# Kernel optimization log

Measured on AMD Instinct MI355X. Metric: run time of the kernel, lower is better.

## Reference

```python
import jax, jax.numpy as jnp
import numpy as np
import math

WINDOW = 14
NUM_HEADS = 12


def setup_inputs() -> dict:
    key = jax.random.key(0)
    k1, k2, k3 = jax.random.split(key, 3)
    B, H, W, C = 8, 80, 80, 768
    x = jax.random.normal(k1, (B, H * W, C), dtype=jnp.float32)
    Wqkv = jax.random.normal(k2, (C, 3 * C), dtype=jnp.float32) * 0.02
    Wproj = jax.random.normal(k3, (C, C), dtype=jnp.float32) * 0.02
    bproj = jnp.zeros((C,), dtype=jnp.float32)
    return {"x": x, "Wqkv": Wqkv, "Wproj": Wproj, "bproj": bproj, "H": H, "W": W}


def reference(x, Wqkv, Wproj, bproj, H, W):
    B, N, C = x.shape
    w = WINDOW
    nh = NUM_HEADS
    hd = C // nh
    scale = hd ** (-0.5)
    Hp = math.ceil(H / w) * w
    Wp = math.ceil(W / w) * w
    nH, nW = Hp // w, Wp // w
    L, Nw = nH * nW, w * w

    qkv = x @ Wqkv                                   # [B, N, 3C]
    grid = qkv.reshape(B, H, W, 3 * C)
    grid = jnp.pad(grid, ((0, 0), (0, Hp - H), (0, Wp - W), (0, 0)))
    # window partition: [B, nH, w, nW, w, 3C] -> [B, L, Nw, 3, nh, hd]
    win = grid.reshape(B, nH, w, nW, w, 3 * C).transpose(0, 1, 3, 2, 4, 5)
    win = win.reshape(B, L, Nw, 3, nh, hd)
    q = win[:, :, :, 0].transpose(0, 1, 3, 2, 4)     # [B, L, nh, Nw, hd]
    k = win[:, :, :, 1].transpose(0, 1, 3, 2, 4)
    v = win[:, :, :, 2].transpose(0, 1, 3, 2, 4)

    attn = jnp.einsum('blhnd,blhmd->blhnm', q, k) * scale
    attn = jax.nn.softmax(attn, axis=-1)
    out = jnp.einsum('blhnm,blhmd->blhnd', attn, v)  # [B, L, nh, Nw, hd]

    # window merge (fold with stride == kernel, non-overlapping)
    out = out.transpose(0, 1, 3, 2, 4).reshape(B, nH, nW, w, w, C)
    out = out.transpose(0, 1, 3, 2, 4, 5).reshape(B, Hp, Wp, C)
    out = out[:, :H, :W, :].reshape(B, N, C)
    return out @ Wproj + bproj
```

## Files before the change

### kernel.cpp

```cpp
#include <hip/hip_runtime.h>

typedef unsigned short u16;
typedef __attribute__((ext_vector_type(4))) float f32x4;
typedef __attribute__((ext_vector_type(8))) short bf16x8;

__device__ __forceinline__ u16 f2bf(float f) {
  unsigned u = __builtin_bit_cast(unsigned, f);
  u += 0x7FFFu + ((u >> 16) & 1u);
  return (u16)(u >> 16);
}

__device__ __forceinline__ void load16(const void* g, void* l) {
  __builtin_amdgcn_global_load_lds((const __attribute__((address_space(1))) void*)g,
                                   (__attribute__((address_space(3))) void*)l, 16, 0, 0);
}

#define LDS_ORDER() do { __builtin_amdgcn_s_waitcnt(0xC07F); asm volatile("" ::: "memory"); } while (0)


__global__ void cvt_x(const float* __restrict__ in, u16* __restrict__ out, int n4) {
  int i = blockIdx.x * 256 + threadIdx.x;
  if (i < n4) {
    float4 v = ((const float4*)in)[i];
    ushort4 o;
    o.x = f2bf(v.x); o.y = f2bf(v.y); o.z = f2bf(v.z); o.w = f2bf(v.w);
    ((ushort4*)out)[i] = o;
  }
}

__global__ void cvt_wt(const float* __restrict__ W, u16* __restrict__ Wt, int K, int N) {
  int idx = blockIdx.x * 256 + threadIdx.x;
  if (idx < N * K) {
    int n = idx / K, k = idx - n * K;
    Wt[idx] = f2bf(W[(size_t)k * N + n]);
  }
}


__global__ __launch_bounds__(256) void gemm_qkv(const u16* __restrict__ A,
                                                const u16* __restrict__ Bt,
                                                u16* __restrict__ qkvP,
                                                int M, int N, int K) {
  __shared__ __align__(16) u16 lA[128 * 32];
  __shared__ __align__(16) u16 lB[128 * 32];
  const int t = threadIdx.x;
  const int lane = t & 63, wave = t >> 6;
  const int wm = wave & 1, wn = wave >> 1;
  const int col = lane & 15, quad = lane >> 4;
  const int bn = blockIdx.x, bm = blockIdx.y;

  const int rowA = t >> 2;
  const int ke = (t & 3) * 8;
  const u16* gA = A + (size_t)(bm * 128 + rowA) * K + ke;
  const u16* gB = Bt + (size_t)(bn * 128 + rowA) * K + ke;
  u16* dA = &lA[t * 8];
  u16* dB = &lB[t * 8];
  const size_t stride64 = (size_t)64 * K;

  f32x4 acc[4][4] = {};

  for (int k0 = 0; k0 < K; k0 += 32) {
    load16(gA + k0, dA);
    load16(gA + k0 + stride64, dA + 2048);
    load16(gB + k0, dB);
    load16(gB + k0 + stride64, dB + 2048);
    __syncthreads();
    bf16x8 af[4], bfr[4];
#pragma unroll
    for (int i = 0; i < 4; i++)
      af[i] = *(const bf16x8*)&lA[(wm * 64 + i * 16 + col) * 32 + quad * 8];
#pragma unroll
    for (int j = 0; j < 4; j++)
      bfr[j] = *(const bf16x8*)&lB[(wn * 64 + j * 16 + col) * 32 + quad * 8];
#pragma unroll
    for (int i = 0; i < 4; i++)
#pragma unroll
      for (int j = 0; j < 4; j++)
        acc[i][j] = __builtin_amdgcn_mfma_f32_16x16x32_bf16(af[i], bfr[j], acc[i][j], 0, 0, 0);
    __syncthreads();
  }

  const int c0 = bn * 128 + wn * 64;
  const int mat = c0 / 768;
  const int hh = (c0 - mat * 768) >> 6;
  const int r0 = bm * 128 + wm * 64 + quad * 4;
#pragma unroll
  for (int i = 0; i < 4; i++) {
#pragma unroll
    for (int r = 0; r < 4; r++) {
      int row = r0 + i * 16 + r;
      int bb = row / 6400;
      int rem = row - bb * 6400;
      int y = rem / 80, x = rem - (rem / 80) * 80;
      int wy = y / 14, wx = x / 14;
      int iy = y - wy * 14, ix = x - wx * 14;
      int win = wy * 6 + wx;
      int kidx = iy * 14 + ix;
      size_t base = ((size_t)((bb * 36 + win) * 3 + mat) * 12 + hh) * 12544 + (size_t)kidx * 64;
#pragma unroll
      for (int j = 0; j < 4; j++)
        qkvP[base + j * 16 + col] = f2bf(acc[i][j][r]);
    }
  }
}


__global__ __launch_bounds__(256) void gemm_proj(const u16* __restrict__ A,
                                                 const u16* __restrict__ Bt,
                                                 float* __restrict__ C,
                                                 const float* __restrict__ bias,
                                                 int M, int N, int K) {
  __shared__ __align__(16) u16 lA[128 * 32];
  __shared__ __align__(16) u16 lB[128 * 32];
  const int t = threadIdx.x;
  const int lane = t & 63, wave = t >> 6;
  const int wm = wave & 1, wn = wave >> 1;
  const int col = lane & 15, quad = lane >> 4;
  const int bn = blockIdx.x, bm = blockIdx.y;

  const int rowA = t >> 2;
  const int ke = (t & 3) * 8;
  const u16* gA = A + (size_t)(bm * 128 + rowA) * K + ke;
  const u16* gB = Bt + (size_t)(bn * 128 + rowA) * K + ke;
  u16* dA = &lA[t * 8];
  u16* dB = &lB[t * 8];
  const size_t stride64 = (size_t)64 * K;

  f32x4 acc[4][4] = {};

  for (int k0 = 0; k0 < K; k0 += 32) {
    load16(gA + k0, dA);
    load16(gA + k0 + stride64, dA + 2048);
    load16(gB + k0, dB);
    load16(gB + k0 + stride64, dB + 2048);
    __syncthreads();
    bf16x8 af[4], bfr[4];
#pragma unroll
    for (int i = 0; i < 4; i++)
      af[i] = *(const bf16x8*)&lA[(wm * 64 + i * 16 + col) * 32 + quad * 8];
#pragma unroll
    for (int j = 0; j < 4; j++)
      bfr[j] = *(const bf16x8*)&lB[(wn * 64 + j * 16 + col) * 32 + quad * 8];
#pragma unroll
    for (int i = 0; i < 4; i++)
#pragma unroll
      for (int j = 0; j < 4; j++)
        acc[i][j] = __builtin_amdgcn_mfma_f32_16x16x32_bf16(af[i], bfr[j], acc[i][j], 0, 0, 0);
    __syncthreads();
  }

  const int r0 = bm * 128 + wm * 64 + quad * 4;
  const int c0 = bn * 128 + wn * 64 + col;
  float bv[4];
#pragma unroll
  for (int j = 0; j < 4; j++) bv[j] = bias[c0 + j * 16];
#pragma unroll
  for (int i = 0; i < 4; i++)
#pragma unroll
    for (int j = 0; j < 4; j++)
#pragma unroll
      for (int r = 0; r < 4; r++)
        C[(size_t)(r0 + i * 16 + r) * N + (c0 + j * 16)] = acc[i][j][r] + bv[j];
}


__global__ __launch_bounds__(256) void win_attn(const u16* __restrict__ qkvP,
                                                u16* __restrict__ out) {
  __shared__ __align__(16) u16 sK[2 * 208 * 32];
  __shared__ __align__(16) u16 sVt[7 * 64 * 32];
  __shared__ __align__(16) u16 sVrow[200 * 64];

  const int h = blockIdx.x;
  const int win = blockIdx.y;
  const int b = blockIdx.z;
  const int wy = win / 6, wx = win - wy * 6;
  const int y0 = wy * 14, x0 = wx * 14;
  const int t = threadIdx.x, wave = t >> 6, lane = t & 63;
  const int colq = lane & 15, quad = lane >> 4;

  const size_t bwin = (size_t)(b * 36 + win) * 3;
  const u16* qbase = qkvP + ((bwin + 0) * 12 + h) * 12544;
  const u16* kbase = qkvP + ((bwin + 1) * 12 + h) * 12544;
  const u16* vbase = qkvP + ((bwin + 2) * 12 + h) * 12544;

  for (int s = t; s < 3264; s += 256) {
    if (s < 1664) {
      int half = s / 832;
      int rem = s - half * 832;
      int row = rem >> 2, e = rem & 3;
      int srow = row < 196 ? row : 0;
      load16(kbase + srow * 64 + half * 32 + e * 8, (u16*)sK + s * 8);
    } else {
      int s2 = s - 1664;
      load16(vbase + s2 * 8, sVrow + s2 * 8);
    }
  }
  __syncthreads();

  const bool boundary = (wx == 5) || (wy == 5);
  for (int jj = t; jj < 14336; jj += 256) {
    int kc = jj >> 11;
    int r2 = jj & 2047;
    int j = r2 >> 6, d = r2 & 63;
    int k = (j + d) & 31;
    int kidx = kc * 32 + k;
    u16 val = 0;
    if (kidx < 196) {
      int iy = kidx / 14, ix = kidx - (kidx / 14) * 14;
      if (y0 + iy < 80 && x0 + ix < 80) val = sVrow[kidx * 64 + d];
    }
    sVt[kc * 2048 + d * 32 + k] = val;
  }
  if (boundary) {
    for (int jj = t; jj < 13312; jj += 256) {
      int row = jj >> 6, d = jj & 63;
      if (row < 196) {
        int iy = row / 14, ix = row - (row / 14) * 14;
        if (y0 + iy >= 80 || x0 + ix >= 80)
          sK[((d >> 5) * 208 + row) * 32 + (d & 31)] = 0;
      }
    }
  }
  __syncthreads();

  u16* sPw = sVrow + wave * 640;

  int mt = wave;
  const u16* qp = qbase + (mt * 16 + colq) * 64 + quad * 8;
  bf16x8 qa0 = *(const bf16x8*)qp;
  bf16x8 qa1 = *(const bf16x8*)(qp + 32);
  while (mt < 13) {
    int mtn = mt + 4;
    bf16x8 qn0 = qa0, qn1 = qa1;
    if (mtn < 13) {
      const u16* qp2 = qbase + (mtn * 16 + colq) * 64 + quad * 8;
      qn0 = *(const bf16x8*)qp2;
      qn1 = *(const bf16x8*)(qp2 + 32);
    }

    f32x4 s[13];
#pragma unroll
    for (int nt = 0; nt < 13; nt++) {
      bf16x8 kb0 = *(const bf16x8*)&sK[(nt * 16 + colq) * 32 + quad * 8];
      bf16x8 kb1 = *(const bf16x8*)&sK[((208 + nt * 16 + colq)) * 32 + quad * 8];
      f32x4 a = {0.f, 0.f, 0.f, 0.f};
      a = __builtin_amdgcn_mfma_f32_16x16x32_bf16(qa0, kb0, a, 0, 0, 0);
      a = __builtin_amdgcn_mfma_f32_16x16x32_bf16(qa1, kb1, a, 0, 0, 0);
      s[nt] = a;
    }

    float mx[4] = {-1e30f, -1e30f, -1e30f, -1e30f};
#pragma unroll
    for (int nt = 0; nt < 13; nt++)
#pragma unroll
      for (int r = 0; r < 4; r++) {
        float v = s[nt][r] * 0.125f;
        if (nt == 12 && colq >= 4) v = -1e30f;
        s[nt][r] = v;
        mx[r] = fmaxf(mx[r], v);
      }
#pragma unroll
    for (int off = 1; off < 16; off <<= 1)
#pragma unroll
      for (int r = 0; r < 4; r++) mx[r] = fmaxf(mx[r], __shfl_xor(mx[r], off));
    float sm[4] = {0.f, 0.f, 0.f, 0.f};
#pragma unroll
    for (int nt = 0; nt < 13; nt++)
#pragma unroll
      for (int r = 0; r < 4; r++) {
        float e = __expf(s[nt][r] - mx[r]);
        s[nt][r] = e;
        sm[r] += e;
      }
#pragma unroll
    for (int off = 1; off < 16; off <<= 1)
#pragma unroll
      for (int r = 0; r < 4; r++) sm[r] += __shfl_xor(sm[r], off);
    float rs[4];
#pragma unroll
    for (int r = 0; r < 4; r++) rs[r] = 1.0f / sm[r];

    f32x4 o[4] = {};
#pragma unroll
    for (int kc = 0; kc < 7; kc++) {
      const int nt0 = kc * 2, nt1 = kc * 2 + 1;
#pragma unroll
      for (int r = 0; r < 4; r++) {
        sPw[(quad * 4 + r) * 36 + colq] = f2bf(s[nt0][r] * rs[r]);
        sPw[(quad * 4 + r) * 36 + 16 + colq] = (nt1 < 13) ? f2bf(s[nt1][r] * rs[r]) : (u16)0;
      }
      LDS_ORDER();
      bf16x8 pa = *(const bf16x8*)&sPw[colq * 36 + quad * 8];
#pragma unroll
      for (int dt = 0; dt < 4; dt++) {
        bf16x8 vb = *(const bf16x8*)&sVt[(kc * 64 + dt * 16 + colq) * 32 + quad * 8];
        o[dt] = __builtin_amdgcn_mfma_f32_16x16x32_bf16(pa, vb, o[dt], 0, 0, 0);
      }
      LDS_ORDER();
    }

#pragma unroll
    for (int r = 0; r < 4; r++) {
      int qr = mt * 16 + quad * 4 + r;
      if (qr < 196) {
        int iy = qr / 14, ix = qr - (qr / 14) * 14;
        int y = y0 + iy, x = x0 + ix;
        if (y < 80 && x < 80) {
          size_t off = ((size_t)(b * 6400 + y * 80 + x)) * 768 + h * 64 + colq;
#pragma unroll
          for (int dt = 0; dt < 4; dt++) out[off + dt * 16] = f2bf(o[dt][r]);
        }
      }
    }
    qa0 = qn0; qa1 = qn1;
    mt = mtn;
  }
}


extern "C" void kernel_launch(void* const* d_in, const int* in_sizes, int n_in,
                              void* d_out, int out_size, void* d_ws, size_t ws_size,
                              hipStream_t stream) {
  const float* x     = (const float*)d_in[0];
  const float* Wqkv  = (const float*)d_in[1];
  const float* Wproj = (const float*)d_in[2];
  const float* bproj = (const float*)d_in[3];

  char* ws = (char*)d_ws;
  const size_t QKVP_BYTES = (size_t)130056192 * 2 + 4096;
  const size_t X_BYTES    = (size_t)51200 * 768 * 2;
  const size_t WQT_BYTES  = (size_t)2304 * 768 * 2;
  u16* qkvP   = (u16*)ws;
  u16* xbf    = (u16*)(ws + QKVP_BYTES);
  u16* wqkvT  = (u16*)(ws + QKVP_BYTES + X_BYTES);
  u16* wprojT = (u16*)(ws + QKVP_BYTES + X_BYTES + WQT_BYTES);
  u16* aout   = xbf;

  cvt_x<<<38400, 256, 0, stream>>>(x, xbf, 9830400);
  cvt_wt<<<6912, 256, 0, stream>>>(Wqkv, wqkvT, 768, 2304);
  cvt_wt<<<2304, 256, 0, stream>>>(Wproj, wprojT, 768, 768);
  gemm_qkv<<<dim3(18, 400), 256, 0, stream>>>(xbf, wqkvT, qkvP, 51200, 2304, 768);
  win_attn<<<dim3(12, 36, 8), 256, 0, stream>>>(qkvP, aout);
  gemm_proj<<<dim3(6, 400), 256, 0, stream>>>(aout, wprojT, (float*)d_out, bproj, 51200, 768, 768);
}
```

Before: 861.8 us.

## Replace QKV and projection GEMMs with 256x256 double-buffered pipelined MFMA core

Both GEMMs now share a 256x256-tile core run by 512 threads. It double-buffers K=64 slices in a 128KB LDS buffer with XOR-swizzled layout and interleaves global-to-LDS prefetch with four MFMA quadrants, using explicit vmcnt/lgkmcnt waits and s_setprio. Block IDs are remapped in groups of 8 to improve L2 locality. The aim is to hide load latency, raise reuse per tile and cut LDS bank conflicts. The cost is higher register and LDS pressure, fewer workgroups, and K hardcoded to 768.

```diff
diff --git a/kernel.cpp b/kernel.cpp
--- a/kernel.cpp
+++ b/kernel.cpp
@@ -16,6 +16,12 @@
 }
 
 #define LDS_ORDER() do { __builtin_amdgcn_s_waitcnt(0xC07F); asm volatile("" ::: "memory"); } while (0)
+
+#define FENCE() asm volatile("" ::: "memory")
+#define BARRIER() do { FENCE(); __builtin_amdgcn_s_barrier(); FENCE(); } while (0)
+#define WAIT_VM2() asm volatile("s_waitcnt vmcnt(2)" ::: "memory")
+#define WAIT_VM0() asm volatile("s_waitcnt vmcnt(0)" ::: "memory")
+#define LGKM0() asm volatile("s_waitcnt lgkmcnt(0)" ::: "memory")
 
 
 __global__ void cvt_x(const float* __restrict__ in, u16* __restrict__ out, int n4) {
@@ -37,58 +43,148 @@
 }
 
 
-__global__ __launch_bounds__(256) void gemm_qkv(const u16* __restrict__ A,
-                                                const u16* __restrict__ Bt,
-                                                u16* __restrict__ qkvP,
-                                                int M, int N, int K) {
-  __shared__ __align__(16) u16 lA[128 * 32];
-  __shared__ __align__(16) u16 lB[128 * 32];
+template <int MB, int NB>
+__device__ __forceinline__ void mfma_quad(f32x4 (&acc)[8][4], const bf16x8 (&af)[4][2],
+                                          const bf16x8 (&bf_)[4][2]) {
+  __builtin_amdgcn_s_setprio(1);
+#pragma unroll
+  for (int mf = 0; mf < 4; mf++)
+#pragma unroll
+    for (int nf = 0; nf < 2; nf++) {
+      acc[MB + mf][NB + nf] = __builtin_amdgcn_mfma_f32_16x16x32_bf16(
+          af[mf][0], bf_[NB + nf][0], acc[MB + mf][NB + nf], 0, 0, 0);
+      acc[MB + mf][NB + nf] = __builtin_amdgcn_mfma_f32_16x16x32_bf16(
+          af[mf][1], bf_[NB + nf][1], acc[MB + mf][NB + nf], 0, 0, 0);
+    }
+  __builtin_amdgcn_s_setprio(0);
+}
+
+__device__ __forceinline__ void mm256_core(const u16* __restrict__ A,
+                                           const u16* __restrict__ Bt,
+                                           int bm, int bn,
+                                           u16* lds, f32x4 (&acc)[8][4]) {
+  const int K = 768;
   const int t = threadIdx.x;
   const int lane = t & 63, wave = t >> 6;
-  const int wm = wave & 1, wn = wave >> 1;
-  const int col = lane & 15, quad = lane >> 4;
-  const int bn = blockIdx.x, bm = blockIdx.y;
-
-  const int rowA = t >> 2;
-  const int ke = (t & 3) * 8;
-  const u16* gA = A + (size_t)(bm * 128 + rowA) * K + ke;
-  const u16* gB = Bt + (size_t)(bn * 128 + rowA) * K + ke;
-  u16* dA = &lA[t * 8];
-  u16* dB = &lB[t * 8];
-  const size_t stride64 = (size_t)64 * K;
-
-  f32x4 acc[4][4] = {};
-
-  for (int k0 = 0; k0 < K; k0 += 32) {
-    load16(gA + k0, dA);
-    load16(gA + k0 + stride64, dA + 2048);
-    load16(gB + k0, dB);
-    load16(gB + k0 + stride64, dB + 2048);
-    __syncthreads();
-    bf16x8 af[4], bfr[4];
-#pragma unroll
-    for (int i = 0; i < 4; i++)
-      af[i] = *(const bf16x8*)&lA[(wm * 64 + i * 16 + col) * 32 + quad * 8];
-#pragma unroll
-    for (int j = 0; j < 4; j++)
-      bfr[j] = *(const bf16x8*)&lB[(wn * 64 + j * 16 + col) * 32 + quad * 8];
-#pragma unroll
-    for (int i = 0; i < 4; i++)
-#pragma unroll
-      for (int j = 0; j < 4; j++)
-        acc[i][j] = __builtin_amdgcn_mfma_f32_16x16x32_bf16(af[i], bfr[j], acc[i][j], 0, 0, 0);
-    __syncthreads();
-  }
-
-  const int c0 = bn * 128 + wn * 64;
-  const int mat = c0 / 768;
-  const int hh = (c0 - mat * 768) >> 6;
-  const int r0 = bm * 128 + wm * 64 + quad * 4;
-#pragma unroll
-  for (int i = 0; i < 4; i++) {
+  const int wm = wave >> 2, wn = wave & 3;
+  const int colq = lane & 15, quad = lane >> 4;
+
+  const u16* Ab = A + (size_t)bm * 256 * K;
+  const u16* Bb = Bt + (size_t)bn * 256 * K;
+
+  u16* const lA = lds;
+  u16* const lB = lds + 32768;
+
+  const int srow = t >> 3;
+  const int gslot = (t & 7) ^ (srow & 7);
+
+#define STAGE_(gb, lb)                                                          \
+  do {                                                                          \
+    load16((gb) + (size_t)srow * K + gslot * 8, (lb) + t * 8);                  \
+    load16((gb) + (size_t)(srow + 64) * K + gslot * 8, (lb) + (t + 512) * 8);   \
+  } while (0)
+#define STAGE_A(jj, h) STAGE_(Ab + (size_t)((h) * 128) * K + (jj) * 64, \
+                              lA + ((jj) & 1) * 16384 + (h) * 8192)
+#define STAGE_B(jj, h) STAGE_(Bb + (size_t)((h) * 128) * K + (jj) * 64, \
+                              lB + ((jj) & 1) * 16384 + (h) * 8192)
+
+  const int arow_lo = wm * 128 + colq;
+  const int brow_lo = wn * 64 + colq;
+  const int swz = (colq & 7) << 3;
+#define RD(buf, row, kk) (*(const bf16x8*)&(buf)[(row) * 64 + (((kk) * 32 + quad * 8) ^ swz)])
+
+  bf16x8 af[4][2], bf_[4][2];
+
+  STAGE_A(0, 0); STAGE_A(0, 1); STAGE_B(0, 0); STAGE_B(0, 1);
+  STAGE_A(1, 0);
+  WAIT_VM2();
+  BARRIER();
+
+#pragma unroll 2
+  for (int j = 0; j < 12; ++j) {
+    const u16* cA = lA + (j & 1) * 16384;
+    const u16* cB = lB + (j & 1) * 16384;
+
+#pragma unroll
+    for (int mf = 0; mf < 4; mf++) {
+      af[mf][0] = RD(cA, arow_lo + mf * 16, 0);
+      af[mf][1] = RD(cA, arow_lo + mf * 16, 1);
+    }
+#pragma unroll
+    for (int nf = 0; nf < 2; nf++) {
+      bf_[nf][0] = RD(cB, brow_lo + nf * 16, 0);
+      bf_[nf][1] = RD(cB, brow_lo + nf * 16, 1);
+    }
+    if (j < 11) STAGE_A(j + 1, 1);
+    BARRIER();
+    mfma_quad<0, 0>(acc, af, bf_);
+    LGKM0();
+    BARRIER();
+
+#pragma unroll
+    for (int nf = 0; nf < 2; nf++) {
+      bf_[2 + nf][0] = RD(cB, brow_lo + (2 + nf) * 16, 0);
+      bf_[2 + nf][1] = RD(cB, brow_lo + (2 + nf) * 16, 1);
+    }
+    if (j < 11) STAGE_B(j + 1, 0);
+    BARRIER();
+    mfma_quad<0, 2>(acc, af, bf_);
+    LGKM0();
+    BARRIER();
+
+#pragma unroll
+    for (int mf = 0; mf < 4; mf++) {
+      af[mf][0] = RD(cA, arow_lo + 64 + mf * 16, 0);
+      af[mf][1] = RD(cA, arow_lo + 64 + mf * 16, 1);
+    }
+    if (j < 11) STAGE_B(j + 1, 1);
+    BARRIER();
+    mfma_quad<4, 0>(acc, af, bf_);
+    LGKM0();
+    BARRIER();
+
+    if (j < 10) STAGE_A(j + 2, 0);
+    BARRIER();
+    mfma_quad<4, 2>(acc, af, bf_);
+    if (j < 10) { WAIT_VM2(); }
+    else if (j < 11) { WAIT_VM0(); }
+    BARRIER();
+  }
+#undef RD
+#undef STAGE_A
+#undef STAGE_B
+#undef STAGE_
+}
+
+
+__global__ __launch_bounds__(512, 2) void gemm_qkv(const u16* __restrict__ A,
+                                                   const u16* __restrict__ Bt,
+                                                   u16* __restrict__ qkvP) {
+  __shared__ __align__(16) u16 lds[65536];
+  const int nx = gridDim.x;
+  const int nwg = nx * gridDim.y;
+  const int bid = blockIdx.y * nx + blockIdx.x;
+  const int cpx = nwg >> 3;
+  const int sid = (bid & 7) * cpx + (bid >> 3);
+  const int bm = sid / nx, bn = sid - bm * nx;
+
+  f32x4 acc[8][4] = {};
+  mm256_core(A, Bt, bm, bn, lds, acc);
+
+  const int t = threadIdx.x;
+  const int lane = t & 63, wave = t >> 6;
+  const int wm = wave >> 2, wn = wave & 3;
+  const int colq = lane & 15, quad = lane >> 4;
+
+  const int c64 = bn * 4 + wn;
+  const int mat = c64 / 12;
+  const int hh = c64 - mat * 12;
+  const int r0 = bm * 256 + wm * 128 + quad * 4;
+#pragma unroll
+  for (int mf = 0; mf < 8; mf++) {
 #pragma unroll
     for (int r = 0; r < 4; r++) {
-      int row = r0 + i * 16 + r;
+      int row = r0 + mf * 16 + r;
       int bb = row / 6400;
       int rem = row - bb * 6400;
       int y = rem / 80, x = rem - (rem / 80) * 80;
@@ -98,69 +194,45 @@
       int kidx = iy * 14 + ix;
       size_t base = ((size_t)((bb * 36 + win) * 3 + mat) * 12 + hh) * 12544 + (size_t)kidx * 64;
 #pragma unroll
-      for (int j = 0; j < 4; j++)
-        qkvP[base + j * 16 + col] = f2bf(acc[i][j][r]);
-    }
-  }
-}
-
-
-__global__ __launch_bounds__(256) void gemm_proj(const u16* __restrict__ A,
-                                                 const u16* __restrict__ Bt,
-                                                 float* __restrict__ C,
-                                                 const float* __restrict__ bias,
-                                                 int M, int N, int K) {
-  __shared__ __align__(16) u16 lA[128 * 32];
-  __shared__ __align__(16) u16 lB[128 * 32];
+      for (int nf = 0; nf < 4; nf++)
+        qkvP[base + nf * 16 + colq] = f2bf(acc[mf][nf][r]);
+    }
+  }
+}
+
+
+__global__ __launch_bounds__(512, 2) void gemm_proj(const u16* __restrict__ A,
+                                                    const u16* __restrict__ Bt,
+                                                    float* __restrict__ C,
+                                                    const float* __restrict__ bias) {
+  __shared__ __align__(16) u16 lds[65536];
+  const int nx = gridDim.x;
+  const int nwg = nx * gridDim.y;
+  const int bid = blockIdx.y * nx + blockIdx.x;
+  const int cpx = nwg >> 3;
+  const int sid = (bid & 7) * cpx + (bid >> 3);
+  const int bm = sid / nx, bn = sid - bm * nx;
+
+  f32x4 acc[8][4] = {};
+  mm256_core(A, Bt, bm, bn, lds, acc);
+
   const int t = threadIdx.x;
   const int lane = t & 63, wave = t >> 6;
-  const int wm = wave & 1, wn = wave >> 1;
-  const int col = lane & 15, quad = lane >> 4;
-  const int bn = blockIdx.x, bm = blockIdx.y;
-
-  const int rowA = t >> 2;
-  const int ke = (t & 3) * 8;
-  const u16* gA = A + (size_t)(bm * 128 + rowA) * K + ke;
-  const u16* gB = Bt + (size_t)(bn * 128 + rowA) * K + ke;
-  u16* dA = &lA[t * 8];
-  u16* dB = &lB[t * 8];
-  const size_t stride64 = (size_t)64 * K;
-
-  f32x4 acc[4][4] = {};
-
-  for (int k0 = 0; k0 < K; k0 += 32) {
-    load16(gA + k0, dA);
-    load16(gA + k0 + stride64, dA + 2048);
-    load16(gB + k0, dB);
-    load16(gB + k0 + stride64, dB + 2048);
-    __syncthreads();
-    bf16x8 af[4], bfr[4];
-#pragma unroll
-    for (int i = 0; i < 4; i++)
-      af[i] = *(const bf16x8*)&lA[(wm * 64 + i * 16 + col) * 32 + quad * 8];
-#pragma unroll
-    for (int j = 0; j < 4; j++)
-      bfr[j] = *(const bf16x8*)&lB[(wn * 64 + j * 16 + col) * 32 + quad * 8];
-#pragma unroll
-    for (int i = 0; i < 4; i++)
-#pragma unroll
-      for (int j = 0; j < 4; j++)
-        acc[i][j] = __builtin_amdgcn_mfma_f32_16x16x32_bf16(af[i], bfr[j], acc[i][j], 0, 0, 0);
-    __syncthreads();
-  }
-
-  const int r0 = bm * 128 + wm * 64 + quad * 4;
-  const int c0 = bn * 128 + wn * 64 + col;
+  const int wm = wave >> 2, wn = wave & 3;
+  const int colq = lane & 15, quad = lane >> 4;
+
+  const int r0 = bm * 256 + wm * 128 + quad * 4;
+  const int c0 = bn * 256 + wn * 64 + colq;
   float bv[4];
 #pragma unroll
-  for (int j = 0; j < 4; j++) bv[j] = bias[c0 + j * 16];
-#pragma unroll
-  for (int i = 0; i < 4; i++)
-#pragma unroll
-    for (int j = 0; j < 4; j++)
+  for (int nf = 0; nf < 4; nf++) bv[nf] = bias[c0 + nf * 16];
+#pragma unroll
+  for (int mf = 0; mf < 8; mf++)
+#pragma unroll
+    for (int nf = 0; nf < 4; nf++)
 #pragma unroll
       for (int r = 0; r < 4; r++)
-        C[(size_t)(r0 + i * 16 + r) * N + (c0 + j * 16)] = acc[i][j][r] + bv[j];
+        C[(size_t)(r0 + mf * 16 + r) * 768 + (c0 + nf * 16)] = acc[mf][nf][r] + bv[nf];
 }
 
 
@@ -339,7 +411,7 @@
   cvt_x<<<38400, 256, 0, stream>>>(x, xbf, 9830400);
   cvt_wt<<<6912, 256, 0, stream>>>(Wqkv, wqkvT, 768, 2304);
   cvt_wt<<<2304, 256, 0, stream>>>(Wproj, wprojT, 768, 768);
-  gemm_qkv<<<dim3(18, 400), 256, 0, stream>>>(xbf, wqkvT, qkvP, 51200, 2304, 768);
+  gemm_qkv<<<dim3(9, 200), 512, 0, stream>>>(xbf, wqkvT, qkvP);
   win_attn<<<dim3(12, 36, 8), 256, 0, stream>>>(qkvP, aout);
-  gemm_proj<<<dim3(6, 400), 256, 0, stream>>>(aout, wprojT, (float*)d_out, bproj, 51200, 768, 768);
-}
+  gemm_proj<<<dim3(3, 200), 512, 0, stream>>>(aout, wprojT, (float*)d_out, bproj);
+}
```

After: 779.6 us. -9.5%, faster.
